# Kernel optimization log

Measured on AMD Instinct MI355X. Metric: run time of the kernel, lower is better.

The kernel has to match this reference:

```python
import jax, jax.numpy as jnp
import numpy as np
import math

S, B, D = 1024, 8, 512
H = 8
HD = D // H
DFF = 2048
NUM_BUCKETS = 32
MAX_DISTANCE = 128
LN_EPS = 1e-5


def setup_inputs() -> dict:
    key = jax.random.key(0)
    ks = jax.random.split(key, 12)
    s = 0.02
    return {
        "x": jax.random.normal(ks[0], (S, B, D), jnp.float32),
        "attn_mask": jnp.zeros((S, S), jnp.float32),
        "in_proj_w": jax.random.normal(ks[1], (3 * D, D), jnp.float32) * s,
        "in_proj_b": jnp.zeros((3 * D,), jnp.float32),
        "out_proj_w": jax.random.normal(ks[2], (D, D), jnp.float32) * s,
        "out_proj_b": jnp.zeros((D,), jnp.float32),
        "lin1_w": jax.random.normal(ks[3], (DFF, D), jnp.float32) * s,
        "lin1_b": jnp.zeros((DFF,), jnp.float32),
        "lin2_w": jax.random.normal(ks[4], (D, DFF), jnp.float32) * s,
        "lin2_b": jnp.zeros((D,), jnp.float32),
        "ln1_w": jnp.ones((D,), jnp.float32),
        "ln1_b": jnp.zeros((D,), jnp.float32),
        "ln2_w": jnp.ones((D,), jnp.float32),
        "ln2_b": jnp.zeros((D,), jnp.float32),
        "rel_emb": jax.random.normal(ks[5], (NUM_BUCKETS, H), jnp.float32) * s,
    }


def _relative_position_bucket(relative_position, num_buckets=NUM_BUCKETS, max_distance=MAX_DISTANCE):
    # bidirectional=True path (encoder)
    nb = num_buckets // 2
    rel_buckets = (relative_position > 0).astype(jnp.int32) * nb
    rp = jnp.abs(relative_position)
    max_exact = nb // 2
    is_small = rp < max_exact
    rp_safe = jnp.maximum(rp, 1)  # avoid log(0); masked by is_small below
    rp_large = max_exact + (
        jnp.log(rp_safe.astype(jnp.float32) / max_exact)
        / math.log(max_distance / max_exact)
        * (nb - max_exact)
    ).astype(jnp.int32)
    rp_large = jnp.minimum(rp_large, nb - 1)
    return rel_buckets + jnp.where(is_small, rp, rp_large)


def _compute_bias(rel_emb, q_len, k_len):
    ctx = jnp.arange(q_len, dtype=jnp.int32)[:, None]
    mem = jnp.arange(k_len, dtype=jnp.int32)[None, :]
    buckets = _relative_position_bucket(mem - ctx)          # [S, S]
    values = rel_emb[buckets]                                # [S, S, H]
    return jnp.transpose(values, (2, 0, 1))                  # [H, S, S]


def _layer_norm(x, w, b):
    mu = jnp.mean(x, axis=-1, keepdims=True)
    var = jnp.mean(jnp.square(x - mu), axis=-1, keepdims=True)
    return (x - mu) * jax.lax.rsqrt(var + LN_EPS) * w + b


def reference(x, attn_mask, in_proj_w, in_proj_b, out_proj_w, out_proj_b,
              lin1_w, lin1_b, lin2_w, lin2_b, ln1_w, ln1_b, ln2_w, ln2_b, rel_emb):
    s, b, d = x.shape
    # qkv projection (torch Linear: y = x W^T + b)
    qkv = x @ in_proj_w.T + in_proj_b                         # [S, B, 3D]
    q, k, v = jnp.split(qkv, 3, axis=-1)

    def to_bhsd(t):
        return jnp.transpose(t.reshape(s, b, H, HD), (1, 2, 0, 3))  # [B, H, S, HD]

    q, k, v = to_bhsd(q), to_bhsd(k), to_bhsd(v)
    scores = jnp.einsum("bhqd,bhkd->bhqk", q, k) / math.sqrt(HD)

    bias = _compute_bias(rel_emb, s, s)                       # [H, S, S]
    mask_bias = attn_mask[None, :, :] + bias                  # [H, S, S]
    attn = jax.nn.softmax(scores + mask_bias[None], axis=-1)  # [B, H, S, S]

    o = jnp.einsum("bhqk,bhkd->bhqd", attn, v)                # [B, H, S, HD]
    o = jnp.transpose(o, (2, 0, 1, 3)).reshape(s, b, d)       # [S, B, D]
    o = o @ out_proj_w.T + out_proj_b

    # post-norm (norm_first=False)
    y = _layer_norm(x + o, ln1_w, ln1_b)
    ff = jax.nn.relu(y @ lin1_w.T + lin1_b) @ lin2_w.T + lin2_b
    return _layer_norm(y + ff, ln2_w, ln2_b)
```

## Files before the change

kernel.cpp:

```cpp
#include <hip/hip_runtime.h>
#include <hip/hip_bf16.h>


#define S_LEN 1024
#define BATCH 8
#define DMODEL 512
#define NHEAD 8
#define HDIM 64
#define DFF 2048
#define NROWS (S_LEN * BATCH)

typedef __bf16 bf16x8 __attribute__((ext_vector_type(8)));
typedef short  s16x4  __attribute__((ext_vector_type(4)));
typedef float  f32x4  __attribute__((ext_vector_type(4)));

__device__ __forceinline__ void gload16(const void* g, void* l) {
    __builtin_amdgcn_global_load_lds(
        (const __attribute__((address_space(1))) void*)g,
        (__attribute__((address_space(3))) void*)l, 16, 0, 0);
}

__device__ __forceinline__ void cast4(const float* __restrict__ src,
                                      __hip_bfloat16* __restrict__ dst, int off) {
    float4 v = *(const float4*)(src + (size_t)off * 4);
    union { s16x4 s; __hip_bfloat16 b[4]; } u;
    u.b[0] = __float2bfloat16(v.x); u.b[1] = __float2bfloat16(v.y);
    u.b[2] = __float2bfloat16(v.z); u.b[3] = __float2bfloat16(v.w);
    *(s16x4*)(dst + (size_t)off * 4) = u.s;
}

__global__ __launch_bounds__(256)
void prep_cast_kernel(const float* __restrict__ x, const float* __restrict__ wq,
                      __hip_bfloat16* __restrict__ xb,
                      __hip_bfloat16* __restrict__ wqb) {
    const int NX = NROWS * DMODEL / 4;
    const int NQ = 3 * DMODEL * DMODEL / 4;
    int i = blockIdx.x * 256 + threadIdx.x;
    if (i < NX)              cast4(x, xb, i);
    else if ((i -= NX) < NQ) cast4(wq, wqb, i);
}

#define TSTR 136

__global__ __launch_bounds__(256, 4)
void qkv_fused(const __hip_bfloat16* __restrict__ Ab,
               const __hip_bfloat16* __restrict__ Wb,
               const float* __restrict__ bias,
               __hip_bfloat16* __restrict__ outq,
               const float* __restrict__ wo, const float* __restrict__ w1,
               const float* __restrict__ w2,
               __hip_bfloat16* __restrict__ wob, __hip_bfloat16* __restrict__ w1b,
               __hip_bfloat16* __restrict__ w2b,
               const float* __restrict__ mask,
               const float* __restrict__ rel_emb,
               __hip_bfloat16* __restrict__ embC) {
    __shared__ __align__(16) __bf16 SH[128 * TSTR];

    if (blockIdx.x < 256) {
        float* ebt = (float*)SH;
        ebt[threadIdx.x] = __expf(rel_emb[threadIdx.x]);
        __syncthreads();
        int t2 = blockIdx.x * 256 + threadIdx.x;
        int qt = t2 >> 12, w = (t2 >> 10) & 3, kb = (t2 >> 6) & 15, lane = t2 & 63;
        int q = qt * 64 + w * 16 + (lane & 15);
        float em[16]; int bv[16];
#pragma unroll
        for (int j = 0; j < 16; ++j) {
            int c = j >> 2, e = j & 3;
            int k = kb * 64 + c * 16 + (lane >> 4) * 4 + e;
            int rel = k - q;
            int bucket = (rel > 0) ? 16 : 0;
            int rp = rel < 0 ? -rel : rel;
            int v;
            if (rp < 8)          v = rp;
            else if (rp < 12)    v = 8;
            else if (rp < 16)    v = 9;
            else if (rp < 23)    v = 10;
            else if (rp < 32)    v = 11;
            else if (rp < 46)    v = 12;
            else if (rp < 64)    v = 13;
            else if (rp < 91)    v = 14;
            else                 v = 15;
            bv[j] = (bucket + v) * NHEAD;
            em[j] = __expf(mask[(size_t)q * S_LEN + k]);
        }
#pragma unroll
        for (int h = 0; h < NHEAD; ++h) {
            __hip_bfloat16 ov[16];
#pragma unroll
            for (int j = 0; j < 16; ++j)
                ov[j] = __float2bfloat16(em[j] * ebt[bv[j] + h]);
            size_t idx = ((((size_t)h * 16 + qt) * 4 + w) * 16 + kb) * 64 + lane;
            *(uint4*)(embC + idx * 16)     = *(uint4*)&ov[0];
            *(uint4*)(embC + idx * 16 + 8) = *(uint4*)&ov[8];
        }
        return;
    }
    if (blockIdx.x >= 1024) {
        const int NO = DMODEL * DMODEL / 4;
        const int N1 = DFF * DMODEL / 4;
        int i = (blockIdx.x - 1024) * 256 + threadIdx.x;
        if (i < NO)              cast4(wo, wob, i);
        else if ((i -= NO) < N1) cast4(w1, w1b, i);
        else                     cast4(w2, w2b, i - N1);
        return;
    }

    const int id = blockIdx.x - 256;
    const int by = id & 63, bx = id >> 6;
    const int w = threadIdx.x >> 6;
    const int lane = threadIdx.x & 63;
    const int m16 = lane & 15;
    const int quad = lane >> 4;
    const int row0 = by * 128;
    const int col0 = bx * 128;
    const int rowbase = (w >> 1) * 64;
    const int colbase = (w & 1) * 64;
    const int K = DMODEL;

    __bf16* As = SH;
    __bf16* Bs = SH + 128 * 64;

    const __bf16* Ap = (const __bf16*)Ab;
    const __bf16* Wp = (const __bf16*)Wb;

    const int a_row_in_grp = lane >> 3;
    const int kb_sw = (lane & 7) ^ (lane >> 3);

    f32x4 acc[4][4];
#pragma unroll
    for (int c = 0; c < 4; ++c)
#pragma unroll
        for (int r = 0; r < 4; ++r) acc[c][r] = f32x4{0, 0, 0, 0};

    for (int k0 = 0; k0 < K; k0 += 64) {
#pragma unroll
        for (int i = 0; i < 4; ++i) {
            int grp = w * 4 + i;
            int row = grp * 8 + a_row_in_grp;
            gload16(Ap + (size_t)(row0 + row) * K + k0 + kb_sw * 8,
                    (void*)(As + grp * 512));
            gload16(Wp + (size_t)(col0 + row) * K + k0 + kb_sw * 8,
                    (void*)(Bs + grp * 512));
        }
        __syncthreads();

#pragma unroll
        for (int kk = 0; kk < 2; ++kk) {
            bf16x8 af[4], bfr[4];
            int slot = (kk * 4 + quad) ^ (m16 & 7);
#pragma unroll
            for (int r = 0; r < 4; ++r)
                af[r] = *(const bf16x8*)(As + (rowbase + r * 16 + m16) * 64 + slot * 8);
#pragma unroll
            for (int c = 0; c < 4; ++c)
                bfr[c] = *(const bf16x8*)(Bs + (colbase + c * 16 + m16) * 64 + slot * 8);
#pragma unroll
            for (int c = 0; c < 4; ++c)
#pragma unroll
                for (int r = 0; r < 4; ++r)
                    acc[c][r] = __builtin_amdgcn_mfma_f32_16x16x32_bf16(
                        af[r], bfr[c], acc[c][r], 0, 0, 0);
        }
        __syncthreads();
    }

    __hip_bfloat16* T = (__hip_bfloat16*)SH;
#pragma unroll
    for (int c = 0; c < 4; ++c) {
        int colL = colbase + c * 16 + m16;
        float bv = bias[col0 + colL];
#pragma unroll
        for (int r = 0; r < 4; ++r) {
            int rowL = rowbase + r * 16 + quad * 4;
#pragma unroll
            for (int e = 0; e < 4; ++e)
                T[(rowL + e) * TSTR + colL] = __float2bfloat16(acc[c][r][e] + bv);
        }
    }
    __syncthreads();

    const int u = threadIdx.x;
    if (col0 < 1024) {
        int rowL = u >> 1, half = u & 1;
        int gcol = col0 + half * 64;
        int sect = gcol >> 9, h = (gcol >> 6) & 7;
        int s = (row0 + rowL) >> 3, bb = (row0 + rowL) & 7;
        size_t base = ((size_t)(sect * 64 + bb * 8 + h) * S_LEN + s) * HDIM;
        __hip_bfloat16* op = outq + base;
#pragma unroll
        for (int j = 0; j < 8; ++j)
            *(uint4*)(op + j * 8) = *(const uint4*)&T[rowL * TSTR + half * 64 + j * 8];
    } else {
#pragma unroll
        for (int t2 = 0; t2 < 4; ++t2) {
            int pairIdx = u * 4 + t2;
            int bb = pairIdx >> 7;
            int cl = pairIdx & 127;
            int gcol = col0 + cl;
            int h = (gcol >> 6) & 7, d = gcol & 63;
            unsigned short tv[16];
#pragma unroll
            for (int k = 0; k < 16; ++k)
                tv[k] = *(const unsigned short*)&T[(bb + 8 * k) * TSTR + cl];
            size_t base = (size_t)(128 + bb * 8 + h) * (S_LEN * HDIM)
                        + (size_t)d * S_LEN + by * 16;
            *(uint4*)(outq + base)     = *(uint4*)&tv[0];
            *(uint4*)(outq + base + 8) = *(uint4*)&tv[8];
        }
    }
}

template <int MODE, bool RELU>
__global__ __launch_bounds__(256, 4)
void gemm_tile(const __hip_bfloat16* __restrict__ Ab,
               const __hip_bfloat16* __restrict__ Wb,
               const float* __restrict__ bias,
               void* __restrict__ outv,
               int N, int M, int Kloop, int Kstride) {
    const int id = blockIdx.x;
    int by, bx, bz;
    if (MODE == 0) { bz = id >> 8; int rem = id & 255; by = rem & 63; bx = rem >> 6; }
    else           { bz = 0; by = id & 63; bx = id >> 6; }
    const int w = threadIdx.x >> 6;
    const int lane = threadIdx.x & 63;
    const int m16 = lane & 15;
    const int quad = lane >> 4;
    const int row0 = by * 128;
    const int col0 = bx * 128;
    const int kbase = bz * Kloop;
    const int rowbase = (w >> 1) * 64;
    const int colbase = (w & 1) * 64;

    __shared__ __align__(16) __bf16 SH[128 * TSTR];
    __bf16* As = SH;
    __bf16* Bs = SH + 128 * 64;

    const __bf16* Ap = (const __bf16*)Ab;
    const __bf16* Wp = (const __bf16*)Wb;

    const int a_row_in_grp = lane >> 3;
    const int kb_sw = (lane & 7) ^ (lane >> 3);

    f32x4 acc[4][4];
#pragma unroll
    for (int c = 0; c < 4; ++c)
#pragma unroll
        for (int r = 0; r < 4; ++r) acc[c][r] = f32x4{0, 0, 0, 0};

    for (int k0 = 0; k0 < Kloop; k0 += 64) {
#pragma unroll
        for (int i = 0; i < 4; ++i) {
            int grp = w * 4 + i;
            int row = grp * 8 + a_row_in_grp;
            gload16(Ap + (size_t)(row0 + row) * Kstride + kbase + k0 + kb_sw * 8,
                    (void*)(As + grp * 512));
            gload16(Wp + (size_t)(col0 + row) * Kstride + kbase + k0 + kb_sw * 8,
                    (void*)(Bs + grp * 512));
        }
        __syncthreads();

#pragma unroll
        for (int kk = 0; kk < 2; ++kk) {
            bf16x8 af[4], bfr[4];
            int slot = (kk * 4 + quad) ^ (m16 & 7);
#pragma unroll
            for (int r = 0; r < 4; ++r)
                af[r] = *(const bf16x8*)(As + (rowbase + r * 16 + m16) * 64 + slot * 8);
#pragma unroll
            for (int c = 0; c < 4; ++c)
                bfr[c] = *(const bf16x8*)(Bs + (colbase + c * 16 + m16) * 64 + slot * 8);
#pragma unroll
            for (int c = 0; c < 4; ++c)
#pragma unroll
                for (int r = 0; r < 4; ++r)
                    acc[c][r] = __builtin_amdgcn_mfma_f32_16x16x32_bf16(
                        af[r], bfr[c], acc[c][r], 0, 0, 0);
        }
        __syncthreads();
    }

    if (MODE == 0) {
#pragma unroll
        for (int c = 0; c < 4; ++c) {
            int col = col0 + colbase + c * 16 + m16;
            float bv = (bz != 0) ? 0.f : bias[col];
#pragma unroll
            for (int r = 0; r < 4; ++r)
#pragma unroll
                for (int e = 0; e < 4; ++e) {
                    int row = row0 + rowbase + r * 16 + quad * 4 + e;
                    ((float*)outv)[(size_t)bz * N * M + (size_t)row * M + col] =
                        acc[c][r][e] + bv;
                }
        }
    } else {
        __hip_bfloat16* T = (__hip_bfloat16*)SH;
#pragma unroll
        for (int c = 0; c < 4; ++c) {
            int colL = colbase + c * 16 + m16;
            float bv = bias[col0 + colL];
#pragma unroll
            for (int r = 0; r < 4; ++r) {
                int rowL = rowbase + r * 16 + quad * 4;
#pragma unroll
                for (int e = 0; e < 4; ++e) {
                    float v = acc[c][r][e] + bv;
                    if (RELU) v = fmaxf(v, 0.f);
                    T[(rowL + e) * TSTR + colL] = __float2bfloat16(v);
                }
            }
        }
        __syncthreads();
        const int u = threadIdx.x;
        int rowL = u >> 1, half = u & 1;
        __hip_bfloat16* op = (__hip_bfloat16*)outv
                           + (size_t)(row0 + rowL) * M + col0 + half * 64;
#pragma unroll
        for (int j = 0; j < 8; ++j)
            *(uint4*)(op + j * 8) = *(const uint4*)&T[rowL * TSTR + half * 64 + j * 8];
    }
}

__global__ __launch_bounds__(256)
void gemm64_db(const __hip_bfloat16* __restrict__ Ab,
               const __hip_bfloat16* __restrict__ Wb,
               const float* __restrict__ bias,
               float* __restrict__ outf,
               int N, int M, int K) {
    const int id = blockIdx.x;
    const int by = id & 63, bx = id >> 6;
    const int w = threadIdx.x >> 6;
    const int lane = threadIdx.x & 63;
    const int m16 = lane & 15;
    const int quad = lane >> 4;
    const int row0 = by * 128;
    const int col0 = bx * 64;
    const int rowbase = w * 32;

    __shared__ __align__(16) __bf16 As[2][128 * 64];
    __shared__ __align__(16) __bf16 Bs[2][64 * 64];

    const __bf16* Ap = (const __bf16*)Ab;
    const __bf16* Wp = (const __bf16*)Wb;

    const int a_row_in_grp = lane >> 3;
    const int kb_sw = (lane & 7) ^ (lane >> 3);

    auto stage = [&](int k0, int p) {
#pragma unroll
        for (int i = 0; i < 4; ++i) {
            int grp = w * 4 + i;
            int row = grp * 8 + a_row_in_grp;
            gload16(Ap + (size_t)(row0 + row) * K + k0 + kb_sw * 8,
                    (void*)(&As[p][grp * 512]));
        }
#pragma unroll
        for (int i = 0; i < 2; ++i) {
            int grp = w * 2 + i;
            int row = grp * 8 + a_row_in_grp;
            gload16(Wp + (size_t)(col0 + row) * K + k0 + kb_sw * 8,
                    (void*)(&Bs[p][grp * 512]));
        }
    };

    f32x4 acc[4][2];
#pragma unroll
    for (int c = 0; c < 4; ++c)
#pragma unroll
        for (int r = 0; r < 2; ++r) acc[c][r] = f32x4{0, 0, 0, 0};

    stage(0, 0);
    __syncthreads();

    int p = 0;
    for (int k0 = 0; k0 < K; k0 += 64, p ^= 1) {
        if (k0 + 64 < K) stage(k0 + 64, p ^ 1);
#pragma unroll
        for (int kk = 0; kk < 2; ++kk) {
            bf16x8 af[2], bfr[4];
            int slot = (kk * 4 + quad) ^ (m16 & 7);
#pragma unroll
            for (int r = 0; r < 2; ++r)
                af[r] = *(const bf16x8*)(&As[p][(rowbase + r * 16 + m16) * 64 + slot * 8]);
#pragma unroll
            for (int c = 0; c < 4; ++c)
                bfr[c] = *(const bf16x8*)(&Bs[p][(c * 16 + m16) * 64 + slot * 8]);
#pragma unroll
            for (int c = 0; c < 4; ++c)
#pragma unroll
                for (int r = 0; r < 2; ++r)
                    acc[c][r] = __builtin_amdgcn_mfma_f32_16x16x32_bf16(
                        af[r], bfr[c], acc[c][r], 0, 0, 0);
        }
        __syncthreads();
    }

#pragma unroll
    for (int c = 0; c < 4; ++c) {
        int col = col0 + c * 16 + m16;
        float bv = bias[col];
#pragma unroll
        for (int r = 0; r < 2; ++r)
#pragma unroll
            for (int e = 0; e < 4; ++e) {
                int row = row0 + rowbase + r * 16 + quad * 4 + e;
                outf[(size_t)row * M + col] = acc[c][r][e] + bv;
            }
    }
}

__global__ __launch_bounds__(256, 2)
void attn_mfma(const __hip_bfloat16* __restrict__ qkv_bhsd,
               const __hip_bfloat16* __restrict__ embC,
               __hip_bfloat16* __restrict__ o) {
    const int id = blockIdx.x;
    const int h = id & 7;
    const int qb = (id >> 3) & 7;
    const int b = id >> 6;
    const int bh = b * 8 + h;
    const int q0 = qb * 128;
    const int t = threadIdx.x;
    const int w = t >> 6, lane = t & 63, m16 = lane & 15, quad = lane >> 4;

    const __bf16* Qb  = (const __bf16*)qkv_bhsd + (size_t)bh * (S_LEN * HDIM);
    const __bf16* Kb  = (const __bf16*)qkv_bhsd + (size_t)(64 + bh) * (S_LEN * HDIM);
    const __bf16* VTg = (const __bf16*)qkv_bhsd + (size_t)(128 + bh) * (S_LEN * HDIM);
    const int qtA = qb * 2, qtB = qtA + 1;
    const __hip_bfloat16* ecA =
        embC + ((((size_t)h * 16 + qtA) * 4 + w) * 16) * 1024 + (size_t)lane * 16;
    const __hip_bfloat16* ecB =
        embC + ((((size_t)h * 16 + qtB) * 4 + w) * 16) * 1024 + (size_t)lane * 16;

    __shared__ __align__(16) __bf16 Ks[2][64 * 64];
    __shared__ __align__(16) __bf16 Vs[2][64 * 64];
    __shared__ __align__(16) __bf16 P[4][2][16 * 64];

    const int r_in = lane >> 3;
    const int kb_sw = (lane & 7) ^ r_in;

    auto stage = [&](int kc, int p) {
#pragma unroll
        for (int i = 0; i < 2; ++i) {
            int grp = w * 2 + i;
            gload16(Kb + (size_t)(kc + grp * 8 + r_in) * HDIM + kb_sw * 8,
                    (void*)(&Ks[p][grp * 512]));
            gload16(VTg + (size_t)(grp * 8 + r_in) * S_LEN + kc + kb_sw * 8,
                    (void*)(&Vs[p][grp * 512]));
        }
    };

    bf16x8 aQ0A, aQ1A, aQ0B, aQ1B;
    {
        const __bf16* qpA = Qb + (size_t)(q0 + w * 16 + m16) * HDIM + quad * 8;
        const __bf16* qpB = qpA + (size_t)64 * HDIM;
        bf16x8 t0 = *(const bf16x8*)qpA;
        bf16x8 t1 = *(const bf16x8*)(qpA + 32);
        bf16x8 t2 = *(const bf16x8*)qpB;
        bf16x8 t3 = *(const bf16x8*)(qpB + 32);
#pragma unroll
        for (int j = 0; j < 8; ++j) {
            t0[j] = (__bf16)((float)t0[j] * 0.125f);
            t1[j] = (__bf16)((float)t1[j] * 0.125f);
            t2[j] = (__bf16)((float)t2[j] * 0.125f);
            t3[j] = (__bf16)((float)t3[j] * 0.125f);
        }
        aQ0A = t0; aQ1A = t1; aQ0B = t2; aQ1B = t3;
    }

    f32x4 accOTA[4] = {f32x4{0,0,0,0}, f32x4{0,0,0,0}, f32x4{0,0,0,0}, f32x4{0,0,0,0}};
    f32x4 accOTB[4] = {f32x4{0,0,0,0}, f32x4{0,0,0,0}, f32x4{0,0,0,0}, f32x4{0,0,0,0}};
    float lpartA = 0.f, lpartB = 0.f;

    stage(0, 0);
    __syncthreads();

    int p = 0;
    for (int kc = 0; kc < S_LEN; kc += 64, p ^= 1) {
        if (kc + 64 < S_LEN) stage(kc + 64, p ^ 1);

        union { uint4 u[2]; __hip_bfloat16 e[16]; } evA, evB;
        evA.u[0] = *(const uint4*)(ecA + (size_t)(kc >> 6) * 1024);
        evA.u[1] = *(const uint4*)(ecA + (size_t)(kc >> 6) * 1024 + 8);
        evB.u[0] = *(const uint4*)(ecB + (size_t)(kc >> 6) * 1024);
        evB.u[1] = *(const uint4*)(ecB + (size_t)(kc >> 6) * 1024 + 8);

        f32x4 accTA[4] = {f32x4{0,0,0,0}, f32x4{0,0,0,0}, f32x4{0,0,0,0}, f32x4{0,0,0,0}};
        f32x4 accTB[4] = {f32x4{0,0,0,0}, f32x4{0,0,0,0}, f32x4{0,0,0,0}, f32x4{0,0,0,0}};
        const int sub = (m16 >> 3) * 512 + (m16 & 7) * 64;
        const int s0 = (quad ^ (m16 & 7)) * 8;
        const int s1 = ((4 + quad) ^ (m16 & 7)) * 8;
#pragma unroll
        for (int c = 0; c < 4; ++c) {
            const __bf16* kr = &Ks[p][c * 1024 + sub];
            bf16x8 b0 = *(const bf16x8*)(kr + s0);
            bf16x8 b1 = *(const bf16x8*)(kr + s1);
            accTA[c] = __builtin_amdgcn_mfma_f32_16x16x32_bf16(b0, aQ0A, accTA[c], 0, 0, 0);
            accTA[c] = __builtin_amdgcn_mfma_f32_16x16x32_bf16(b1, aQ1A, accTA[c], 0, 0, 0);
            accTB[c] = __builtin_amdgcn_mfma_f32_16x16x32_bf16(b0, aQ0B, accTB[c], 0, 0, 0);
            accTB[c] = __builtin_amdgcn_mfma_f32_16x16x32_bf16(b1, aQ1B, accTB[c], 0, 0, 0);
        }

#pragma unroll
        for (int c = 0; c < 4; ++c) {
            union { s16x4 s; __hip_bfloat16 bb[4]; } uA, uB;
#pragma unroll
            for (int e = 0; e < 4; ++e) {
                float pvA = __expf(accTA[c][e]) * __bfloat162float(evA.e[c * 4 + e]);
                float pvB = __expf(accTB[c][e]) * __bfloat162float(evB.e[c * 4 + e]);
                lpartA += pvA; lpartB += pvB;
                uA.bb[e] = __float2bfloat16(pvA);
                uB.bb[e] = __float2bfloat16(pvB);
            }
            int blk = (c * 2 + (quad >> 1)) ^ (m16 & 7);
            *(s16x4*)&P[w][0][m16 * 64 + blk * 8 + (quad & 1) * 4] = uA.s;
            *(s16x4*)&P[w][1][m16 * 64 + blk * 8 + (quad & 1) * 4] = uB.s;
        }

        bf16x8 pb0A = *(const bf16x8*)&P[w][0][m16 * 64 + ((quad) ^ (m16 & 7)) * 8];
        bf16x8 pb1A = *(const bf16x8*)&P[w][0][m16 * 64 + ((4 + quad) ^ (m16 & 7)) * 8];
        bf16x8 pb0B = *(const bf16x8*)&P[w][1][m16 * 64 + ((quad) ^ (m16 & 7)) * 8];
        bf16x8 pb1B = *(const bf16x8*)&P[w][1][m16 * 64 + ((4 + quad) ^ (m16 & 7)) * 8];

#pragma unroll
        for (int dt = 0; dt < 4; ++dt) {
            const __bf16* vr = &Vs[p][dt * 1024 + sub];
            bf16x8 v0 = *(const bf16x8*)(vr + s0);
            bf16x8 v1 = *(const bf16x8*)(vr + s1);
            accOTA[dt] = __builtin_amdgcn_mfma_f32_16x16x32_bf16(v0, pb0A, accOTA[dt], 0, 0, 0);
            accOTA[dt] = __builtin_amdgcn_mfma_f32_16x16x32_bf16(v1, pb1A, accOTA[dt], 0, 0, 0);
            accOTB[dt] = __builtin_amdgcn_mfma_f32_16x16x32_bf16(v0, pb0B, accOTB[dt], 0, 0, 0);
            accOTB[dt] = __builtin_amdgcn_mfma_f32_16x16x32_bf16(v1, pb1B, accOTB[dt], 0, 0, 0);
        }

        __syncthreads();
    }

    float lA = lpartA, lB = lpartB;
    lA += __shfl_xor(lA, 16); lA += __shfl_xor(lA, 32);
    lB += __shfl_xor(lB, 16); lB += __shfl_xor(lB, 32);
    float invA = 1.f / lA, invB = 1.f / lB;

    {
        __bf16* Tw = &P[w][0][0];
        const int qr = lane >> 2, ch = lane & 3;
#pragma unroll
        for (int tile = 0; tile < 2; ++tile) {
            const f32x4* accp = tile ? accOTB : accOTA;
            float inv = tile ? invB : invA;
#pragma unroll
            for (int dt = 0; dt < 4; ++dt) {
                union { s16x4 s; __hip_bfloat16 bb4[4]; } uu;
#pragma unroll
                for (int e = 0; e < 4; ++e)
                    uu.bb4[e] = __float2bfloat16(accp[dt][e] * inv);
                *(s16x4*)&Tw[m16 * 72 + dt * 16 + quad * 4] = uu.s;
            }
            asm volatile("s_waitcnt lgkmcnt(0)" ::: "memory");
            __builtin_amdgcn_sched_barrier(0);
            int qg = q0 + tile * 64 + w * 16 + qr;
            __hip_bfloat16* op = o + ((size_t)qg * BATCH + b) * DMODEL
                               + h * HDIM + ch * 16;
            *(uint4*)op       = *(const uint4*)&Tw[qr * 72 + ch * 16];
            *(uint4*)(op + 8) = *(const uint4*)&Tw[qr * 72 + ch * 16 + 8];
            asm volatile("s_waitcnt lgkmcnt(0)" ::: "memory");
            __builtin_amdgcn_sched_barrier(0);
        }
    }
}

__global__ __launch_bounds__(256)
void ln_kernel(const float* __restrict__ resid,
               const float* __restrict__ gin,
               const float* __restrict__ gin2,
               const float* __restrict__ w,
               const float* __restrict__ b,
               float* __restrict__ outf,
               __hip_bfloat16* __restrict__ outb) {
    const int row = blockIdx.x * 4 + (threadIdx.x >> 6);
    const int lane = threadIdx.x & 63;
    const float* rp = resid + (size_t)row * DMODEL;
    const float* gp = gin + (size_t)row * DMODEL;

    float4 v[2];
    float s = 0.f, s2 = 0.f;
#pragma unroll
    for (int i = 0; i < 2; ++i) {
        int d = i * 256 + lane * 4;
        float4 a = *(const float4*)(rp + d);
        float4 g = *(const float4*)(gp + d);
        a.x += g.x; a.y += g.y; a.z += g.z; a.w += g.w;
        if (gin2) {
            float4 g2 = *(const float4*)(gin2 + (size_t)row * DMODEL + d);
            a.x += g2.x; a.y += g2.y; a.z += g2.z; a.w += g2.w;
        }
        v[i] = a;
        s += a.x + a.y + a.z + a.w;
        s2 += a.x * a.x + a.y * a.y + a.z * a.z + a.w * a.w;
    }
#pragma unroll
    for (int off = 32; off; off >>= 1) {
        s  += __shfl_xor(s, off);
        s2 += __shfl_xor(s2, off);
    }
    float mu = s * (1.f / DMODEL);
    float var = s2 * (1.f / DMODEL) - mu * mu;
    float rs = rsqrtf(var + 1e-5f);
#pragma unroll
    for (int i = 0; i < 2; ++i) {
        int d = i * 256 + lane * 4;
        float4 wv = *(const float4*)(w + d);
        float4 bv = *(const float4*)(b + d);
        float4 y;
        y.x = (v[i].x - mu) * rs * wv.x + bv.x;
        y.y = (v[i].y - mu) * rs * wv.y + bv.y;
        y.z = (v[i].z - mu) * rs * wv.z + bv.z;
        y.w = (v[i].w - mu) * rs * wv.w + bv.w;
        *(float4*)(outf + (size_t)row * DMODEL + d) = y;
        if (outb) {
            union { s16x4 s4; __hip_bfloat16 e[4]; } u;
            u.e[0] = __float2bfloat16(y.x); u.e[1] = __float2bfloat16(y.y);
            u.e[2] = __float2bfloat16(y.z); u.e[3] = __float2bfloat16(y.w);
            *(s16x4*)(outb + (size_t)row * DMODEL + d) = u.s4;
        }
    }
}

extern "C" void kernel_launch(void* const* d_in, const int* in_sizes, int n_in,
                              void* d_out, int out_size, void* d_ws, size_t ws_size,
                              hipStream_t stream) {
    const float* x          = (const float*)d_in[0];
    const float* attn_mask  = (const float*)d_in[1];
    const float* in_proj_w  = (const float*)d_in[2];
    const float* in_proj_b  = (const float*)d_in[3];
    const float* out_proj_w = (const float*)d_in[4];
    const float* out_proj_b = (const float*)d_in[5];
    const float* lin1_w     = (const float*)d_in[6];
    const float* lin1_b     = (const float*)d_in[7];
    const float* lin2_w     = (const float*)d_in[8];
    const float* lin2_b     = (const float*)d_in[9];
    const float* ln1_w      = (const float*)d_in[10];
    const float* ln1_b      = (const float*)d_in[11];
    const float* ln2_w      = (const float*)d_in[12];
    const float* ln2_b      = (const float*)d_in[13];
    const float* rel_emb    = (const float*)d_in[14];

    char* ws = (char*)d_ws;
    size_t off = 0;
    auto alloc = [&](size_t bytes) {
        char* p = ws + off;
        off += (bytes + 255) / 256 * 256;
        return (void*)p;
    };
    __hip_bfloat16* embt  = (__hip_bfloat16*)alloc((size_t)NHEAD * S_LEN * S_LEN * 2);
    __hip_bfloat16* wqkvb = (__hip_bfloat16*)alloc((size_t)3 * DMODEL * DMODEL * 2);
    __hip_bfloat16* wob   = (__hip_bfloat16*)alloc((size_t)DMODEL * DMODEL * 2);
    __hip_bfloat16* w1b   = (__hip_bfloat16*)alloc((size_t)DFF * DMODEL * 2);
    __hip_bfloat16* w2b   = (__hip_bfloat16*)alloc((size_t)DMODEL * DFF * 2);
    __hip_bfloat16* xb    = (__hip_bfloat16*)alloc((size_t)NROWS * DMODEL * 2);
    __hip_bfloat16* qkvb  = (__hip_bfloat16*)alloc((size_t)3 * 64 * S_LEN * HDIM * 2);
    __hip_bfloat16* o     = (__hip_bfloat16*)alloc((size_t)NROWS * DMODEL * 2);
    float* tmp            = (float*)alloc((size_t)2 * NROWS * DMODEL * 4);
    float* yf             = (float*)alloc((size_t)NROWS * DMODEL * 4);
    __hip_bfloat16* yb    = (__hip_bfloat16*)alloc((size_t)NROWS * DMODEL * 2);
    __hip_bfloat16* ffb   = (__hip_bfloat16*)alloc((size_t)NROWS * DFF * 2);

    float* out = (float*)d_out;
    float* tmp2 = tmp + (size_t)NROWS * DMODEL;

    prep_cast_kernel<<<dim3(4864), 256, 0, stream>>>(x, in_proj_w, xb, wqkvb);

    qkv_fused<<<dim3(3328), 256, 0, stream>>>(
        xb, wqkvb, in_proj_b, qkvb,
        out_proj_w, lin1_w, lin2_w, wob, w1b, w2b,
        attn_mask, rel_emb, embt);

    attn_mfma<<<dim3(512), 256, 0, stream>>>(qkvb, embt, o);

    gemm64_db<<<dim3(512), 256, 0, stream>>>(
        o, wob, out_proj_b, tmp, NROWS, DMODEL, DMODEL);

    ln_kernel<<<dim3(NROWS / 4), 256, 0, stream>>>(
        x, tmp, nullptr, ln1_w, ln1_b, yf, yb);

    gemm_tile<1, true><<<dim3(1024), 256, 0, stream>>>(
        yb, w1b, lin1_b, ffb, NROWS, DFF, DMODEL, DMODEL);

    gemm_tile<0, false><<<dim3(512), 256, 0, stream>>>(
        ffb, w2b, lin2_b, tmp, NROWS, DMODEL, DFF / 2, DFF);

    ln_kernel<<<dim3(NROWS / 4), 256, 0, stream>>>(
        yf, tmp, tmp2, ln2_w, ln2_b, out, nullptr);
}
```

Measured before the change: 250.7 us.

## Halve attention query tile per block, double grid, compute row sums via MFMA

The attention kernel now handles 64 query rows per block instead of 128 and launches 1024 blocks with a higher occupancy hint, trading reuse of each staged K/V tile for more parallelism and lower register pressure. The row-sum of probabilities is computed with an extra MFMA against a vector of ones instead of per-lane scalar accumulation and shuffles. The precomputed bias table now stores additive mask+relative bias, and exp is applied to score plus bias rather than multiplying by precomputed exponentials. The output transpose staging reuses the K shared buffer, which shrinks shared memory. K/V tiles are now loaded twice as often per head, which raises global/L2 traffic.

Result: slower. 258.4 us (+3.1%).

```diff
diff --git a/kernel.cpp b/kernel.cpp
--- a/kernel.cpp
+++ b/kernel.cpp
@@ -57,8 +57,8 @@
     __shared__ __align__(16) __bf16 SH[128 * TSTR];
 
     if (blockIdx.x < 256) {
-        float* ebt = (float*)SH;
-        ebt[threadIdx.x] = __expf(rel_emb[threadIdx.x]);
+        float* rt = (float*)SH;
+        rt[threadIdx.x] = rel_emb[threadIdx.x];
         __syncthreads();
         int t2 = blockIdx.x * 256 + threadIdx.x;
         int qt = t2 >> 12, w = (t2 >> 10) & 3, kb = (t2 >> 6) & 15, lane = t2 & 63;
@@ -82,14 +82,14 @@
             else if (rp < 91)    v = 14;
             else                 v = 15;
             bv[j] = (bucket + v) * NHEAD;
-            em[j] = __expf(mask[(size_t)q * S_LEN + k]);
+            em[j] = mask[(size_t)q * S_LEN + k];
         }
 #pragma unroll
         for (int h = 0; h < NHEAD; ++h) {
             __hip_bfloat16 ov[16];
 #pragma unroll
             for (int j = 0; j < 16; ++j)
-                ov[j] = __float2bfloat16(em[j] * ebt[bv[j] + h]);
+                ov[j] = __float2bfloat16(em[j] + rt[bv[j] + h]);
             size_t idx = ((((size_t)h * 16 + qt) * 4 + w) * 16 + kb) * 64 + lane;
             *(uint4*)(embC + idx * 16)     = *(uint4*)&ov[0];
             *(uint4*)(embC + idx * 16 + 8) = *(uint4*)&ov[8];
@@ -410,31 +410,28 @@
     }
 }
 
-__global__ __launch_bounds__(256, 2)
+__global__ __launch_bounds__(256, 4)
 void attn_mfma(const __hip_bfloat16* __restrict__ qkv_bhsd,
                const __hip_bfloat16* __restrict__ embC,
                __hip_bfloat16* __restrict__ o) {
     const int id = blockIdx.x;
     const int h = id & 7;
-    const int qb = (id >> 3) & 7;
-    const int b = id >> 6;
+    const int qb = (id >> 3) & 15;
+    const int b = id >> 7;
     const int bh = b * 8 + h;
-    const int q0 = qb * 128;
+    const int q0 = qb * 64;
     const int t = threadIdx.x;
     const int w = t >> 6, lane = t & 63, m16 = lane & 15, quad = lane >> 4;
 
     const __bf16* Qb  = (const __bf16*)qkv_bhsd + (size_t)bh * (S_LEN * HDIM);
     const __bf16* Kb  = (const __bf16*)qkv_bhsd + (size_t)(64 + bh) * (S_LEN * HDIM);
     const __bf16* VTg = (const __bf16*)qkv_bhsd + (size_t)(128 + bh) * (S_LEN * HDIM);
-    const int qtA = qb * 2, qtB = qtA + 1;
-    const __hip_bfloat16* ecA =
-        embC + ((((size_t)h * 16 + qtA) * 4 + w) * 16) * 1024 + (size_t)lane * 16;
-    const __hip_bfloat16* ecB =
-        embC + ((((size_t)h * 16 + qtB) * 4 + w) * 16) * 1024 + (size_t)lane * 16;
+    const __hip_bfloat16* ec =
+        embC + ((((size_t)h * 16 + qb) * 4 + w) * 16) * 1024 + (size_t)lane * 16;
 
     __shared__ __align__(16) __bf16 Ks[2][64 * 64];
     __shared__ __align__(16) __bf16 Vs[2][64 * 64];
-    __shared__ __align__(16) __bf16 P[4][2][16 * 64];
+    __shared__ __align__(16) __bf16 P[4][16 * 64];
 
     const int r_in = lane >> 3;
     const int kb_sw = (lane & 7) ^ r_in;
@@ -450,27 +447,25 @@
         }
     };
 
-    bf16x8 aQ0A, aQ1A, aQ0B, aQ1B;
+    bf16x8 aQ0, aQ1;
     {
-        const __bf16* qpA = Qb + (size_t)(q0 + w * 16 + m16) * HDIM + quad * 8;
-        const __bf16* qpB = qpA + (size_t)64 * HDIM;
-        bf16x8 t0 = *(const bf16x8*)qpA;
-        bf16x8 t1 = *(const bf16x8*)(qpA + 32);
-        bf16x8 t2 = *(const bf16x8*)qpB;
-        bf16x8 t3 = *(const bf16x8*)(qpB + 32);
+        const __bf16* qp = Qb + (size_t)(q0 + w * 16 + m16) * HDIM + quad * 8;
+        bf16x8 t0 = *(const bf16x8*)qp;
+        bf16x8 t1 = *(const bf16x8*)(qp + 32);
 #pragma unroll
         for (int j = 0; j < 8; ++j) {
             t0[j] = (__bf16)((float)t0[j] * 0.125f);
             t1[j] = (__bf16)((float)t1[j] * 0.125f);
-            t2[j] = (__bf16)((float)t2[j] * 0.125f);
-            t3[j] = (__bf16)((float)t3[j] * 0.125f);
-        }
-        aQ0A = t0; aQ1A = t1; aQ0B = t2; aQ1B = t3;
-    }
-
-    f32x4 accOTA[4] = {f32x4{0,0,0,0}, f32x4{0,0,0,0}, f32x4{0,0,0,0}, f32x4{0,0,0,0}};
-    f32x4 accOTB[4] = {f32x4{0,0,0,0}, f32x4{0,0,0,0}, f32x4{0,0,0,0}, f32x4{0,0,0,0}};
-    float lpartA = 0.f, lpartB = 0.f;
+        }
+        aQ0 = t0; aQ1 = t1;
+    }
+
+    union { bf16x8 v; unsigned short us[8]; } vone;
+#pragma unroll
+    for (int j = 0; j < 8; ++j) vone.us[j] = 0x3F80;
+
+    f32x4 accOT[4] = {f32x4{0,0,0,0}, f32x4{0,0,0,0}, f32x4{0,0,0,0}, f32x4{0,0,0,0}};
+    f32x4 accL = f32x4{0, 0, 0, 0};
 
     stage(0, 0);
     __syncthreads();
@@ -479,14 +474,11 @@
     for (int kc = 0; kc < S_LEN; kc += 64, p ^= 1) {
         if (kc + 64 < S_LEN) stage(kc + 64, p ^ 1);
 
-        union { uint4 u[2]; __hip_bfloat16 e[16]; } evA, evB;
-        evA.u[0] = *(const uint4*)(ecA + (size_t)(kc >> 6) * 1024);
-        evA.u[1] = *(const uint4*)(ecA + (size_t)(kc >> 6) * 1024 + 8);
-        evB.u[0] = *(const uint4*)(ecB + (size_t)(kc >> 6) * 1024);
-        evB.u[1] = *(const uint4*)(ecB + (size_t)(kc >> 6) * 1024 + 8);
-
-        f32x4 accTA[4] = {f32x4{0,0,0,0}, f32x4{0,0,0,0}, f32x4{0,0,0,0}, f32x4{0,0,0,0}};
-        f32x4 accTB[4] = {f32x4{0,0,0,0}, f32x4{0,0,0,0}, f32x4{0,0,0,0}, f32x4{0,0,0,0}};
+        union { uint4 u[2]; __hip_bfloat16 e[16]; } ev;
+        ev.u[0] = *(const uint4*)(ec + (size_t)(kc >> 6) * 1024);
+        ev.u[1] = *(const uint4*)(ec + (size_t)(kc >> 6) * 1024 + 8);
+
+        f32x4 accT[4] = {f32x4{0,0,0,0}, f32x4{0,0,0,0}, f32x4{0,0,0,0}, f32x4{0,0,0,0}};
         const int sub = (m16 >> 3) * 512 + (m16 & 7) * 64;
         const int s0 = (quad ^ (m16 & 7)) * 8;
         const int s1 = ((4 + quad) ^ (m16 & 7)) * 8;
@@ -495,77 +487,60 @@
             const __bf16* kr = &Ks[p][c * 1024 + sub];
             bf16x8 b0 = *(const bf16x8*)(kr + s0);
             bf16x8 b1 = *(const bf16x8*)(kr + s1);
-            accTA[c] = __builtin_amdgcn_mfma_f32_16x16x32_bf16(b0, aQ0A, accTA[c], 0, 0, 0);
-            accTA[c] = __builtin_amdgcn_mfma_f32_16x16x32_bf16(b1, aQ1A, accTA[c], 0, 0, 0);
-            accTB[c] = __builtin_amdgcn_mfma_f32_16x16x32_bf16(b0, aQ0B, accTB[c], 0, 0, 0);
-            accTB[c] = __builtin_amdgcn_mfma_f32_16x16x32_bf16(b1, aQ1B, accTB[c], 0, 0, 0);
+            accT[c] = __builtin_amdgcn_mfma_f32_16x16x32_bf16(b0, aQ0, accT[c], 0, 0, 0);
+            accT[c] = __builtin_amdgcn_mfma_f32_16x16x32_bf16(b1, aQ1, accT[c], 0, 0, 0);
         }
 
 #pragma unroll
         for (int c = 0; c < 4; ++c) {
-            union { s16x4 s; __hip_bfloat16 bb[4]; } uA, uB;
+            union { s16x4 s; __hip_bfloat16 bb[4]; } u4;
 #pragma unroll
             for (int e = 0; e < 4; ++e) {
-                float pvA = __expf(accTA[c][e]) * __bfloat162float(evA.e[c * 4 + e]);
-                float pvB = __expf(accTB[c][e]) * __bfloat162float(evB.e[c * 4 + e]);
-                lpartA += pvA; lpartB += pvB;
-                uA.bb[e] = __float2bfloat16(pvA);
-                uB.bb[e] = __float2bfloat16(pvB);
+                float evf = __bfloat162float(ev.e[c * 4 + e]);
+                float pv = __expf(accT[c][e] + evf);
+                u4.bb[e] = __float2bfloat16(pv);
             }
             int blk = (c * 2 + (quad >> 1)) ^ (m16 & 7);
-            *(s16x4*)&P[w][0][m16 * 64 + blk * 8 + (quad & 1) * 4] = uA.s;
-            *(s16x4*)&P[w][1][m16 * 64 + blk * 8 + (quad & 1) * 4] = uB.s;
-        }
-
-        bf16x8 pb0A = *(const bf16x8*)&P[w][0][m16 * 64 + ((quad) ^ (m16 & 7)) * 8];
-        bf16x8 pb1A = *(const bf16x8*)&P[w][0][m16 * 64 + ((4 + quad) ^ (m16 & 7)) * 8];
-        bf16x8 pb0B = *(const bf16x8*)&P[w][1][m16 * 64 + ((quad) ^ (m16 & 7)) * 8];
-        bf16x8 pb1B = *(const bf16x8*)&P[w][1][m16 * 64 + ((4 + quad) ^ (m16 & 7)) * 8];
+            *(s16x4*)&P[w][m16 * 64 + blk * 8 + (quad & 1) * 4] = u4.s;
+        }
+
+        bf16x8 pb0 = *(const bf16x8*)&P[w][m16 * 64 + ((quad) ^ (m16 & 7)) * 8];
+        bf16x8 pb1 = *(const bf16x8*)&P[w][m16 * 64 + ((4 + quad) ^ (m16 & 7)) * 8];
 
 #pragma unroll
         for (int dt = 0; dt < 4; ++dt) {
             const __bf16* vr = &Vs[p][dt * 1024 + sub];
             bf16x8 v0 = *(const bf16x8*)(vr + s0);
             bf16x8 v1 = *(const bf16x8*)(vr + s1);
-            accOTA[dt] = __builtin_amdgcn_mfma_f32_16x16x32_bf16(v0, pb0A, accOTA[dt], 0, 0, 0);
-            accOTA[dt] = __builtin_amdgcn_mfma_f32_16x16x32_bf16(v1, pb1A, accOTA[dt], 0, 0, 0);
-            accOTB[dt] = __builtin_amdgcn_mfma_f32_16x16x32_bf16(v0, pb0B, accOTB[dt], 0, 0, 0);
-            accOTB[dt] = __builtin_amdgcn_mfma_f32_16x16x32_bf16(v1, pb1B, accOTB[dt], 0, 0, 0);
-        }
-
-        __syncthreads();
-    }
-
-    float lA = lpartA, lB = lpartB;
-    lA += __shfl_xor(lA, 16); lA += __shfl_xor(lA, 32);
-    lB += __shfl_xor(lB, 16); lB += __shfl_xor(lB, 32);
-    float invA = 1.f / lA, invB = 1.f / lB;
+            accOT[dt] = __builtin_amdgcn_mfma_f32_16x16x32_bf16(v0, pb0, accOT[dt], 0, 0, 0);
+            accOT[dt] = __builtin_amdgcn_mfma_f32_16x16x32_bf16(v1, pb1, accOT[dt], 0, 0, 0);
+        }
+        accL = __builtin_amdgcn_mfma_f32_16x16x32_bf16(vone.v, pb0, accL, 0, 0, 0);
+        accL = __builtin_amdgcn_mfma_f32_16x16x32_bf16(vone.v, pb1, accL, 0, 0, 0);
+
+        __syncthreads();
+    }
+
+    const float inv = 1.f / accL[0];
 
     {
-        __bf16* Tw = &P[w][0][0];
+        __bf16* Tw = ((__bf16*)Ks) + (size_t)w * 1152;
+#pragma unroll
+        for (int dt = 0; dt < 4; ++dt) {
+            union { s16x4 s; __hip_bfloat16 bb4[4]; } uu;
+#pragma unroll
+            for (int e = 0; e < 4; ++e)
+                uu.bb4[e] = __float2bfloat16(accOT[dt][e] * inv);
+            *(s16x4*)&Tw[m16 * 72 + dt * 16 + quad * 4] = uu.s;
+        }
+        asm volatile("s_waitcnt lgkmcnt(0)" ::: "memory");
+        __builtin_amdgcn_sched_barrier(0);
         const int qr = lane >> 2, ch = lane & 3;
-#pragma unroll
-        for (int tile = 0; tile < 2; ++tile) {
-            const f32x4* accp = tile ? accOTB : accOTA;
-            float inv = tile ? invB : invA;
-#pragma unroll
-            for (int dt = 0; dt < 4; ++dt) {
-                union { s16x4 s; __hip_bfloat16 bb4[4]; } uu;
-#pragma unroll
-                for (int e = 0; e < 4; ++e)
-                    uu.bb4[e] = __float2bfloat16(accp[dt][e] * inv);
-                *(s16x4*)&Tw[m16 * 72 + dt * 16 + quad * 4] = uu.s;
-            }
-            asm volatile("s_waitcnt lgkmcnt(0)" ::: "memory");
-            __builtin_amdgcn_sched_barrier(0);
-            int qg = q0 + tile * 64 + w * 16 + qr;
-            __hip_bfloat16* op = o + ((size_t)qg * BATCH + b) * DMODEL
-                               + h * HDIM + ch * 16;
-            *(uint4*)op       = *(const uint4*)&Tw[qr * 72 + ch * 16];
-            *(uint4*)(op + 8) = *(const uint4*)&Tw[qr * 72 + ch * 16 + 8];
-            asm volatile("s_waitcnt lgkmcnt(0)" ::: "memory");
-            __builtin_amdgcn_sched_barrier(0);
-        }
+        int qg = q0 + w * 16 + qr;
+        __hip_bfloat16* op = o + ((size_t)qg * BATCH + b) * DMODEL
+                           + h * HDIM + ch * 16;
+        *(uint4*)op       = *(const uint4*)&Tw[qr * 72 + ch * 16];
+        *(uint4*)(op + 8) = *(const uint4*)&Tw[qr * 72 + ch * 16 + 8];
     }
 }
 
@@ -675,7 +650,7 @@
         out_proj_w, lin1_w, lin2_w, wob, w1b, w2b,
         attn_mask, rel_emb, embt);
 
-    attn_mfma<<<dim3(512), 256, 0, stream>>>(qkvb, embt, o);
+    attn_mfma<<<dim3(1024), 256, 0, stream>>>(qkvb, embt, o);
 
     gemm64_db<<<dim3(512), 256, 0, stream>>>(
         o, wob, out_proj_b, tmp, NROWS, DMODEL, DMODEL);
```
